# Kernel tuning notes

Hardware: AMD Instinct MI355X
Metric: run time of the kernel (lower is better)

## Reference

```python
import jax, jax.numpy as jnp
import numpy as np

SQRT2 = 1.4142135623730951

def _oyzx2spin():
    # 0yzx -> (uu, ud, du, dd) spin projection matrix, complex64
    M = np.array([[1, 0, 1, 0],
                  [0, -1j, 0, 1],
                  [0, 1j, 0, 1],
                  [1, 0, -1, 0]], dtype=np.complex64) / SQRT2
    return jnp.asarray(M)


def setup_inputs() -> dict:
    key = jax.random.key(0)
    B, C_real, nL, nR = 65536, 8, 13, 13  # C_real = 2 * C_complex (soc_complex_doubling), C_complex % 4 == 0
    HR_in = jax.random.normal(key, (B, C_real, nL, nR), dtype=jnp.float32)
    return {"HR_in": HR_in}


def reference(HR_in):
    # Faithful translation of E3Hamiltonian._spin_projection with
    # real storage + soc_complex_doubling=True.
    B, C_real, nL, nR = HR_in.shape
    half = C_real // 2  # complex channel count
    # pack complex-doubled real storage into complex channels
    HR_c = jax.lax.complex(HR_in[:, :half], HR_in[:, half:])  # [B, half, nL, nR] complex
    n_chunks = half // 4
    HR_view = HR_c.reshape(B, n_chunks, 4, nL, nR)  # 4 = (0, y, z, x) spin components
    M = _oyzx2spin()  # [4(spin), 4(0yzx)]
    # project 0yzx components onto (uu, ud, du, dd) spin basis
    HR_proj = jnp.einsum('nkslr,ps->nkplr', HR_view, M)
    HR_proj_flat = HR_proj.reshape(B, half, nL, nR)
    # unpack back to real storage: [real-half | imag-half] along channel dim
    return jnp.concatenate([HR_proj_flat.real, HR_proj_flat.imag], axis=1)
```

## Files before the change

### kernel.cpp

```cpp
#include <hip/hip_runtime.h>


#define PLANE 169
#define CSTRIDE 1352
#define IPB 4
#define SLAB_F (IPB * CSTRIDE)
#define SLAB_V (SLAB_F / 4)
#define SITES (IPB * PLANE)

__global__ __launch_bounds__(256) void spin_proj_kernel(
    const float4* __restrict__ in, float4* __restrict__ out) {
    __shared__ float lds[SLAB_F];
    float4* lds4 = (float4*)lds;

    const size_t base = (size_t)blockIdx.x * SLAB_V;
    const int t = threadIdx.x;

    #pragma unroll
    for (int k = 0; k < 6; ++k) {
        int v = t + k * 256;
        if (v < SLAB_V) lds4[v] = in[base + v];
    }
    __syncthreads();

    float vals[3][8];
    #pragma unroll
    for (int k = 0; k < 3; ++k) {
        int s = t + k * 256;
        if (s < SITES) {
            int item = s / PLANE;
            int j = s - item * PLANE;
            const float* p = lds + item * CSTRIDE + j;
            #pragma unroll
            for (int c = 0; c < 8; ++c) vals[k][c] = p[c * PLANE];
        }
    }
    __syncthreads();

    const float sc = 0.70710678118654752440f;
    #pragma unroll
    for (int k = 0; k < 3; ++k) {
        int s = t + k * 256;
        if (s < SITES) {
            int item = s / PLANE;
            int j = s - item * PLANE;
            float* p = lds + item * CSTRIDE + j;
            float r0 = vals[k][0], r1 = vals[k][1], r2 = vals[k][2], r3 = vals[k][3];
            float i0 = vals[k][4], i1 = vals[k][5], i2 = vals[k][6], i3 = vals[k][7];
            p[0 * PLANE] = (r0 + r2) * sc;
            p[1 * PLANE] = (i1 + r3) * sc;
            p[2 * PLANE] = (r3 - i1) * sc;
            p[3 * PLANE] = (r0 - r2) * sc;
            p[4 * PLANE] = (i0 + i2) * sc;
            p[5 * PLANE] = (i3 - r1) * sc;
            p[6 * PLANE] = (r1 + i3) * sc;
            p[7 * PLANE] = (i0 - i2) * sc;
        }
    }
    __syncthreads();

    #pragma unroll
    for (int k = 0; k < 6; ++k) {
        int v = t + k * 256;
        if (v < SLAB_V) out[base + v] = lds4[v];
    }
}

extern "C" void kernel_launch(void* const* d_in, const int* in_sizes, int n_in,
                              void* d_out, int out_size, void* d_ws, size_t ws_size,
                              hipStream_t stream) {
    const float4* in = (const float4*)d_in[0];
    float4* out = (float4*)d_out;

    int n_items = in_sizes[0] / CSTRIDE;
    int grid = n_items / IPB;
    spin_proj_kernel<<<grid, 256, 0, stream>>>(in, out);
}
```

Before: 138.5 us.

## Assign one item per wavefront and replace block barriers with wave-local sync

Each wavefront now owns a single item's LDS slab and does its own load, in-place projection and store, so the three block-wide __syncthreads become wave-level waitcnt plus wave barriers. The intermediate register staging pass and the extra barrier that separated reads from writes are removed, since each lane now reads and writes only its own sites. The aim is to let waves progress independently and cut barrier stalls in this memory-bound kernel. In exchange, lane utilisation is uneven: 169 sites per 64-lane wave leaves part of the third iteration idle.

```diff
diff --git a/kernel.cpp b/kernel.cpp
--- a/kernel.cpp
+++ b/kernel.cpp
@@ -3,66 +3,60 @@
 
 #define PLANE 169
 #define CSTRIDE 1352
-#define IPB 4
-#define SLAB_F (IPB * CSTRIDE)
-#define SLAB_V (SLAB_F / 4)
-#define SITES (IPB * PLANE)
+#define QUADS 338
+#define WAVES 4
 
 __global__ __launch_bounds__(256) void spin_proj_kernel(
     const float4* __restrict__ in, float4* __restrict__ out) {
-    __shared__ float lds[SLAB_F];
-    float4* lds4 = (float4*)lds;
+    __shared__ float lds[WAVES * CSTRIDE];
 
-    const size_t base = (size_t)blockIdx.x * SLAB_V;
-    const int t = threadIdx.x;
+    const int wave = threadIdx.x >> 6;
+    const int lane = threadIdx.x & 63;
+    float* slab = lds + wave * CSTRIDE;
+    float4* slab4 = (float4*)slab;
+
+    const size_t item = (size_t)blockIdx.x * WAVES + wave;
+    const float4* __restrict__ gin = in + item * QUADS;
+    float4* __restrict__ gout = out + item * QUADS;
 
     #pragma unroll
     for (int k = 0; k < 6; ++k) {
-        int v = t + k * 256;
-        if (v < SLAB_V) lds4[v] = in[base + v];
+        int v = lane + k * 64;
+        if (v < QUADS) slab4[v] = gin[v];
     }
-    __syncthreads();
-
-    float vals[3][8];
-    #pragma unroll
-    for (int k = 0; k < 3; ++k) {
-        int s = t + k * 256;
-        if (s < SITES) {
-            int item = s / PLANE;
-            int j = s - item * PLANE;
-            const float* p = lds + item * CSTRIDE + j;
-            #pragma unroll
-            for (int c = 0; c < 8; ++c) vals[k][c] = p[c * PLANE];
-        }
-    }
-    __syncthreads();
+    asm volatile("s_waitcnt lgkmcnt(0)" ::: "memory");
+    __builtin_amdgcn_wave_barrier();
 
     const float sc = 0.70710678118654752440f;
     #pragma unroll
     for (int k = 0; k < 3; ++k) {
-        int s = t + k * 256;
-        if (s < SITES) {
-            int item = s / PLANE;
-            int j = s - item * PLANE;
-            float* p = lds + item * CSTRIDE + j;
-            float r0 = vals[k][0], r1 = vals[k][1], r2 = vals[k][2], r3 = vals[k][3];
-            float i0 = vals[k][4], i1 = vals[k][5], i2 = vals[k][6], i3 = vals[k][7];
-            p[0 * PLANE] = (r0 + r2) * sc;
-            p[1 * PLANE] = (i1 + r3) * sc;
-            p[2 * PLANE] = (r3 - i1) * sc;
-            p[3 * PLANE] = (r0 - r2) * sc;
-            p[4 * PLANE] = (i0 + i2) * sc;
-            p[5 * PLANE] = (i3 - r1) * sc;
-            p[6 * PLANE] = (r1 + i3) * sc;
-            p[7 * PLANE] = (i0 - i2) * sc;
+        int j = lane + k * 64;
+        if (j < PLANE) {
+            float r0 = slab[0 * PLANE + j];
+            float r1 = slab[1 * PLANE + j];
+            float r2 = slab[2 * PLANE + j];
+            float r3 = slab[3 * PLANE + j];
+            float i0 = slab[4 * PLANE + j];
+            float i1 = slab[5 * PLANE + j];
+            float i2 = slab[6 * PLANE + j];
+            float i3 = slab[7 * PLANE + j];
+            slab[0 * PLANE + j] = (r0 + r2) * sc;
+            slab[1 * PLANE + j] = (i1 + r3) * sc;
+            slab[2 * PLANE + j] = (r3 - i1) * sc;
+            slab[3 * PLANE + j] = (r0 - r2) * sc;
+            slab[4 * PLANE + j] = (i0 + i2) * sc;
+            slab[5 * PLANE + j] = (i3 - r1) * sc;
+            slab[6 * PLANE + j] = (r1 + i3) * sc;
+            slab[7 * PLANE + j] = (i0 - i2) * sc;
         }
     }
-    __syncthreads();
+    asm volatile("s_waitcnt lgkmcnt(0)" ::: "memory");
+    __builtin_amdgcn_wave_barrier();
 
     #pragma unroll
     for (int k = 0; k < 6; ++k) {
-        int v = t + k * 256;
-        if (v < SLAB_V) out[base + v] = lds4[v];
+        int v = lane + k * 64;
+        if (v < QUADS) gout[v] = slab4[v];
     }
 }
 
@@ -73,6 +67,6 @@
     float4* out = (float4*)d_out;
 
     int n_items = in_sizes[0] / CSTRIDE;
-    int grid = n_items / IPB;
+    int grid = n_items / WAVES;
     spin_proj_kernel<<<grid, 256, 0, stream>>>(in, out);
 }
```

Result: faster. 134.6 us (-2.8%).
